# Performance work log

Hardware: AMD Instinct MI355X
Metric: run time of the kernel (lower is better)

Reference implementation:

```python
import jax, jax.numpy as jnp
import numpy as np

N = 8192      # nodes
E = 262144    # edges (avg degree 32)
IN_DIM = 512
H1 = 256
H2 = 128


def _graph_conv(x, src, dst, W, b, act):
    """DGL GraphConv with norm='both', allow_zero_in_degree=True.
    h = D_in^{-1/2} * A @ (D_out^{-1/2} * x @ W) + b, then activation.
    Degrees clamped to min 1 (DGL behavior)."""
    ones = jnp.ones((src.shape[0],), dtype=x.dtype)
    deg_out = jax.ops.segment_sum(ones, src, num_segments=N)
    deg_in = jax.ops.segment_sum(ones, dst, num_segments=N)
    norm_src = jnp.maximum(deg_out, 1.0) ** -0.5  # [N]
    norm_dst = jnp.maximum(deg_in, 1.0) ** -0.5   # [N]
    # apply weight before aggregation (out_feats < in_feats, as DGL does)
    h = (x * norm_src[:, None]) @ W               # [N, out]
    agg = jax.ops.segment_sum(h[src], dst, num_segments=N)  # gather-scatter SpMM
    return act(agg * norm_dst[:, None] + b)


def setup_inputs() -> dict:
    key = jax.random.key(0)
    ks = jax.random.split(key, 7)
    features = jax.random.normal(ks[0], (N, IN_DIM), dtype=jnp.float32)
    src = jax.random.randint(ks[1], (E,), 0, N)
    dst = jax.random.randint(ks[2], (E,), 0, N)
    W1 = jax.random.normal(ks[3], (IN_DIM, H1), dtype=jnp.float32) * (1.0 / np.sqrt(IN_DIM))
    b1 = jnp.zeros((H1,), dtype=jnp.float32)
    W2 = jax.random.normal(ks[4], (H1, H2), dtype=jnp.float32) * (1.0 / np.sqrt(H1))
    b2 = jnp.zeros((H2,), dtype=jnp.float32)
    return {"features": features, "src": src, "dst": dst,
            "W1": W1, "b1": b1, "W2": W2, "b2": b2}


def reference(features, src, dst, W1, b1, W2, b2):
    x = _graph_conv(features, src, dst, W1, b1, jax.nn.relu)
    emb = _graph_conv(x, src, dst, W2, b2, lambda a: a)
    logits = jax.nn.sigmoid(emb @ emb.T)  # [N, N] dense reconstruction
    return (emb, logits)
```

## Files before the change

### kernel.cpp

```cpp
#include <hip/hip_runtime.h>

#define NN 8192
#define EE 262144
#define IN_DIM 512
#define HD1 256
#define HD2 128

typedef __attribute__((ext_vector_type(8))) short bf16x8;
typedef __attribute__((ext_vector_type(4))) float f32x4;

__device__ inline unsigned short f2bf(float f) {
    unsigned int u = __builtin_bit_cast(unsigned int, f);
    u += 0x7fffu + ((u >> 16) & 1u);
    return (unsigned short)(u >> 16);
}


__global__ void deg_kernel(const int* __restrict__ src, const int* __restrict__ dst,
                           int* __restrict__ deg_out, int* __restrict__ deg_in) {
    int e = blockIdx.x * blockDim.x + threadIdx.x;
    if (e < EE) {
        atomicAdd(&deg_out[src[e]], 1);
        atomicAdd(&deg_in[dst[e]], 1);
    }
}

__global__ void norm_kernel(const int* __restrict__ deg_out, const int* __restrict__ deg_in,
                            float* __restrict__ norm_src, float* __restrict__ norm_dst) {
    int i = blockIdx.x * blockDim.x + threadIdx.x;
    if (i < NN) {
        int dout = deg_out[i]; if (dout < 1) dout = 1;
        int din  = deg_in[i];  if (din  < 1) din  = 1;
        norm_src[i] = rsqrtf((float)dout);
        norm_dst[i] = rsqrtf((float)din);
    }
}

__global__ void scan_kernel(const int* __restrict__ counts, int* __restrict__ row_start) {
    __shared__ int sums[256];
    int t = threadIdx.x;
    int base = t * 32;
    int local[32];
    int s = 0;
    for (int i = 0; i < 32; i++) { local[i] = s; s += counts[base + i]; }
    sums[t] = s;
    __syncthreads();
    for (int off = 1; off < 256; off <<= 1) {
        int v = (t >= off) ? sums[t - off] : 0;
        __syncthreads();
        sums[t] += v;
        __syncthreads();
    }
    int coff = (t == 0) ? 0 : sums[t - 1];
    for (int i = 0; i < 32; i++) row_start[base + i] = coff + local[i];
    if (t == 255) row_start[NN] = sums[255];
}

__global__ void fill_kernel(const int* __restrict__ src, const int* __restrict__ dst,
                            const int* __restrict__ row_start, int* __restrict__ cursor,
                            int* __restrict__ eidx) {
    int e = blockIdx.x * blockDim.x + threadIdx.x;
    if (e < EE) {
        int d = dst[e];
        int pos = atomicAdd(&cursor[d], 1);
        eidx[row_start[d] + pos] = src[e];
    }
}


__global__ void scale_cast_kernel(const float4* __restrict__ x, const float* __restrict__ norm_src,
                                  ushort4* __restrict__ out) {
    int idx = blockIdx.x * blockDim.x + threadIdx.x;
    if (idx < NN * IN_DIM / 4) {
        float ns = norm_src[idx >> 7];
        float4 v = x[idx];
        ushort4 o;
        o.x = f2bf(v.x * ns); o.y = f2bf(v.y * ns);
        o.z = f2bf(v.z * ns); o.w = f2bf(v.w * ns);
        out[idx] = o;
    }
}

__global__ void transpose_cast_kernel(const float* __restrict__ W, unsigned short* __restrict__ Wt,
                                      int K, int Nc) {
    int idx = blockIdx.x * blockDim.x + threadIdx.x;
    if (idx < K * Nc) {
        int n = idx / K;
        int k = idx - n * K;
        Wt[idx] = f2bf(W[k * Nc + n]);
    }
}

template <int EPI>
__global__ __launch_bounds__(256) void gemm_tn(const short* __restrict__ A,
                                               const short* __restrict__ B,
                                               float* __restrict__ C, int N, int K) {
    __shared__ float lds[64][132];
    int wave = threadIdx.x >> 6;
    int lane = threadIdx.x & 63;
    int wr = wave >> 1, wc = wave & 1;
    int row0 = blockIdx.y * 128 + wr * 64;
    int col0 = blockIdx.x * 128 + wc * 64;
    int l15 = lane & 15, q = lane >> 4;

    f32x4 acc[4][4] = {};
    const short* Abase = A + (size_t)(row0 + l15) * K + q * 8;
    const short* Bbase = B + (size_t)(col0 + l15) * K + q * 8;
    int nk = K >> 5;
    for (int ks = 0; ks < nk; ks++) {
        bf16x8 a[4], b[4];
#pragma unroll
        for (int t = 0; t < 4; t++) {
            a[t] = *(const bf16x8*)(Abase + (size_t)t * 16 * K + ks * 32);
            b[t] = *(const bf16x8*)(Bbase + (size_t)t * 16 * K + ks * 32);
        }
#pragma unroll
        for (int ti = 0; ti < 4; ti++)
#pragma unroll
            for (int tj = 0; tj < 4; tj++)
                acc[ti][tj] = __builtin_amdgcn_mfma_f32_16x16x32_bf16(a[ti], b[tj], acc[ti][tj], 0, 0, 0);
    }

    int brow = blockIdx.y * 128;
    int bcol = blockIdx.x * 128;
#pragma unroll
    for (int h = 0; h < 2; h++) {
        __syncthreads();
        if (wr == h) {
#pragma unroll
            for (int ti = 0; ti < 4; ti++)
#pragma unroll
                for (int tj = 0; tj < 4; tj++)
#pragma unroll
                    for (int r = 0; r < 4; r++)
                        lds[ti * 16 + q * 4 + r][wc * 64 + tj * 16 + l15] = acc[ti][tj][r];
        }
        __syncthreads();
#pragma unroll
        for (int it = 0; it < 8; it++) {
            int idx = it * 256 + threadIdx.x;
            int rl = idx >> 5;
            int c4 = (idx & 31) << 2;
            f32x4 v = *(const f32x4*)&lds[rl][c4];
            float* dst = C + (size_t)(brow + h * 64 + rl) * N + bcol + c4;
            if (EPI == 1) {
                f32x4 s;
                s[0] = __builtin_amdgcn_rcpf(1.0f + __expf(-v[0]));
                s[1] = __builtin_amdgcn_rcpf(1.0f + __expf(-v[1]));
                s[2] = __builtin_amdgcn_rcpf(1.0f + __expf(-v[2]));
                s[3] = __builtin_amdgcn_rcpf(1.0f + __expf(-v[3]));
                __builtin_nontemporal_store(s, (f32x4*)dst);
            } else {
                *(f32x4*)dst = v;
            }
        }
    }
}


__global__ __launch_bounds__(256) void spmm1_kernel(
        const float* __restrict__ h1, const int* __restrict__ row_start,
        const int* __restrict__ eidx, const float* __restrict__ norm_dst,
        const float* __restrict__ norm_src, const float* __restrict__ b1,
        unsigned short* __restrict__ x1n) {
    int wave = threadIdx.x >> 6, lane = threadIdx.x & 63;
    int r = blockIdx.x * 4 + wave;
    int s = row_start[r], e = row_start[r + 1];
    const float* hb = h1 + (size_t)lane * 4;
    float sx = 0.f, sy = 0.f, sz = 0.f, sw = 0.f;
    int i = s;
    for (; i + 4 <= e; i += 4) {
        int n0 = eidx[i], n1 = eidx[i + 1], n2 = eidx[i + 2], n3 = eidx[i + 3];
        float4 v0 = *(const float4*)(hb + (size_t)n0 * HD1);
        float4 v1 = *(const float4*)(hb + (size_t)n1 * HD1);
        float4 v2 = *(const float4*)(hb + (size_t)n2 * HD1);
        float4 v3 = *(const float4*)(hb + (size_t)n3 * HD1);
        sx += (v0.x + v1.x) + (v2.x + v3.x);
        sy += (v0.y + v1.y) + (v2.y + v3.y);
        sz += (v0.z + v1.z) + (v2.z + v3.z);
        sw += (v0.w + v1.w) + (v2.w + v3.w);
    }
    for (; i < e; i++) {
        float4 v = *(const float4*)(hb + (size_t)eidx[i] * HD1);
        sx += v.x; sy += v.y; sz += v.z; sw += v.w;
    }
    float nd = norm_dst[r], ns = norm_src[r];
    float4 bb = *(const float4*)(b1 + lane * 4);
    ushort4 o;
    o.x = f2bf(fmaxf(sx * nd + bb.x, 0.f) * ns);
    o.y = f2bf(fmaxf(sy * nd + bb.y, 0.f) * ns);
    o.z = f2bf(fmaxf(sz * nd + bb.z, 0.f) * ns);
    o.w = f2bf(fmaxf(sw * nd + bb.w, 0.f) * ns);
    *(ushort4*)(x1n + (size_t)r * HD1 + lane * 4) = o;
}

__global__ __launch_bounds__(256) void spmm2_kernel(
        const float* __restrict__ h2, const int* __restrict__ row_start,
        const int* __restrict__ eidx, const float* __restrict__ norm_dst,
        const float* __restrict__ b2, float* __restrict__ emb,
        unsigned short* __restrict__ embb) {
    int wave = threadIdx.x >> 6, lane = threadIdx.x & 63;
    int r = blockIdx.x * 4 + wave;
    int s = row_start[r], e = row_start[r + 1];
    const float* hb = h2 + (size_t)lane * 2;
    float sx = 0.f, sy = 0.f;
    int i = s;
    for (; i + 4 <= e; i += 4) {
        int n0 = eidx[i], n1 = eidx[i + 1], n2 = eidx[i + 2], n3 = eidx[i + 3];
        float2 v0 = *(const float2*)(hb + (size_t)n0 * HD2);
        float2 v1 = *(const float2*)(hb + (size_t)n1 * HD2);
        float2 v2 = *(const float2*)(hb + (size_t)n2 * HD2);
        float2 v3 = *(const float2*)(hb + (size_t)n3 * HD2);
        sx += (v0.x + v1.x) + (v2.x + v3.x);
        sy += (v0.y + v1.y) + (v2.y + v3.y);
    }
    for (; i < e; i++) {
        float2 v = *(const float2*)(hb + (size_t)eidx[i] * HD2);
        sx += v.x; sy += v.y;
    }
    float nd = norm_dst[r];
    float2 bb = *(const float2*)(b2 + lane * 2);
    float x0 = sx * nd + bb.x;
    float x1 = sy * nd + bb.y;
    float2 ov; ov.x = x0; ov.y = x1;
    *(float2*)(emb + (size_t)r * HD2 + lane * 2) = ov;
    ushort2 ob; ob.x = f2bf(x0); ob.y = f2bf(x1);
    *(ushort2*)(embb + (size_t)r * HD2 + lane * 2) = ob;
}


extern "C" void kernel_launch(void* const* d_in, const int* in_sizes, int n_in,
                              void* d_out, int out_size, void* d_ws, size_t ws_size,
                              hipStream_t stream) {
    const float* features = (const float*)d_in[0];
    const int* src = (const int*)d_in[1];
    const int* dst = (const int*)d_in[2];
    const float* W1 = (const float*)d_in[3];
    const float* b1 = (const float*)d_in[4];
    const float* W2 = (const float*)d_in[5];
    const float* b2 = (const float*)d_in[6];

    char* ws = (char*)d_ws;
    size_t o = 0;
    auto alloc = [&](size_t bytes) -> char* {
        char* p = ws + o;
        o = (o + bytes + 255) & ~(size_t)255;
        return p;
    };
    int* deg_out = (int*)alloc(NN * 4);
    int* deg_in  = (int*)alloc(NN * 4);
    int* cursor  = (int*)alloc(NN * 4);
    float* norm_src = (float*)alloc(NN * 4);
    float* norm_dst = (float*)alloc(NN * 4);
    int* row_start  = (int*)alloc((NN + 1) * 4);
    int* eidx       = (int*)alloc(EE * 4);
    unsigned short* xn  = (unsigned short*)alloc((size_t)NN * IN_DIM * 2);
    unsigned short* w1t = (unsigned short*)alloc((size_t)HD1 * IN_DIM * 2);
    unsigned short* w2t = (unsigned short*)alloc((size_t)HD2 * HD1 * 2);
    float* h1 = (float*)alloc((size_t)NN * HD1 * 4);
    unsigned short* x1n = (unsigned short*)alloc((size_t)NN * HD1 * 2);
    float* h2 = (float*)alloc((size_t)NN * HD2 * 4);
    unsigned short* embb = (unsigned short*)alloc((size_t)NN * HD2 * 2);

    float* emb_out = (float*)d_out;
    float* logits_out = emb_out + (size_t)NN * HD2;

    (void)hipMemsetAsync(deg_out, 0, (size_t)NN * 4 * 3, stream);

    deg_kernel<<<EE / 256, 256, 0, stream>>>(src, dst, deg_out, deg_in);
    norm_kernel<<<NN / 256, 256, 0, stream>>>(deg_out, deg_in, norm_src, norm_dst);
    scan_kernel<<<1, 256, 0, stream>>>(deg_in, row_start);
    fill_kernel<<<EE / 256, 256, 0, stream>>>(src, dst, row_start, cursor, eidx);

    scale_cast_kernel<<<(NN * IN_DIM / 4) / 256, 256, 0, stream>>>(
        (const float4*)features, norm_src, (ushort4*)xn);
    transpose_cast_kernel<<<(IN_DIM * HD1 + 255) / 256, 256, 0, stream>>>(W1, w1t, IN_DIM, HD1);
    transpose_cast_kernel<<<(HD1 * HD2 + 255) / 256, 256, 0, stream>>>(W2, w2t, HD1, HD2);

    gemm_tn<0><<<dim3(HD1 / 128, NN / 128), 256, 0, stream>>>(
        (const short*)xn, (const short*)w1t, h1, HD1, IN_DIM);
    spmm1_kernel<<<NN / 4, 256, 0, stream>>>(h1, row_start, eidx, norm_dst, norm_src, b1, x1n);

    gemm_tn<0><<<dim3(HD2 / 128, NN / 128), 256, 0, stream>>>(
        (const short*)x1n, (const short*)w2t, h2, HD2, HD1);
    spmm2_kernel<<<NN / 4, 256, 0, stream>>>(h2, row_start, eidx, norm_dst, b2, emb_out, embb);

    gemm_tn<1><<<dim3(NN / 128, NN / 128), 256, 0, stream>>>(
        (const short*)embb, (const short*)embb, logits_out, NN, HD2);
}
```

Baseline: 428.5 us.

## Fuse preprocessing kernels and fold feature scaling into first GEMM

Merges degree counting with the weight transpose-casts into one launch, and merges norm computation into the scan kernel. The first GEMM now reads fp32 features directly, converts to bf16 in-register and applies the per-row source norm in the epilogue, which removes the separate scale/cast pass and its intermediate buffer. The small GEMMs use 64-row tiles to launch more blocks on the narrow outputs. Scaling after the bf16 rounding instead of before changes rounding slightly, and the in-loop fp32 loads double the A-operand traffic of GEMM1.

```diff
diff --git a/kernel.cpp b/kernel.cpp
--- a/kernel.cpp
+++ b/kernel.cpp
@@ -15,34 +15,44 @@
     return (unsigned short)(u >> 16);
 }
 
-
-__global__ void deg_kernel(const int* __restrict__ src, const int* __restrict__ dst,
-                           int* __restrict__ deg_out, int* __restrict__ deg_in) {
-    int e = blockIdx.x * blockDim.x + threadIdx.x;
-    if (e < EE) {
+__global__ void prep1_kernel(const int* __restrict__ src, const int* __restrict__ dst,
+                             int* __restrict__ deg_out, int* __restrict__ deg_in,
+                             const float* __restrict__ W1, unsigned short* __restrict__ w1t,
+                             const float* __restrict__ W2, unsigned short* __restrict__ w2t) {
+    int b = blockIdx.x;
+    if (b < 1024) {
+        int e = b * 256 + threadIdx.x;
         atomicAdd(&deg_out[src[e]], 1);
         atomicAdd(&deg_in[dst[e]], 1);
-    }
-}
-
-__global__ void norm_kernel(const int* __restrict__ deg_out, const int* __restrict__ deg_in,
-                            float* __restrict__ norm_src, float* __restrict__ norm_dst) {
-    int i = blockIdx.x * blockDim.x + threadIdx.x;
-    if (i < NN) {
-        int dout = deg_out[i]; if (dout < 1) dout = 1;
-        int din  = deg_in[i];  if (din  < 1) din  = 1;
-        norm_src[i] = rsqrtf((float)dout);
-        norm_dst[i] = rsqrtf((float)din);
-    }
-}
-
-__global__ void scan_kernel(const int* __restrict__ counts, int* __restrict__ row_start) {
+    } else if (b < 1536) {
+        int idx = (b - 1024) * 256 + threadIdx.x;
+        int n = idx / IN_DIM;
+        int k = idx - n * IN_DIM;
+        w1t[idx] = f2bf(W1[k * HD1 + n]);
+    } else {
+        int idx = (b - 1536) * 256 + threadIdx.x;
+        int n = idx / HD1;
+        int k = idx - n * HD1;
+        w2t[idx] = f2bf(W2[k * HD2 + n]);
+    }
+}
+
+__global__ void scan_norm_kernel(const int* __restrict__ deg_in, const int* __restrict__ deg_out,
+                                 int* __restrict__ row_start,
+                                 float* __restrict__ norm_src, float* __restrict__ norm_dst) {
     __shared__ int sums[256];
     int t = threadIdx.x;
     int base = t * 32;
     int local[32];
     int s = 0;
-    for (int i = 0; i < 32; i++) { local[i] = s; s += counts[base + i]; }
+    for (int i = 0; i < 32; i++) {
+        int c = deg_in[base + i];
+        local[i] = s; s += c;
+        int din = (c < 1) ? 1 : c;
+        int dout = deg_out[base + i]; if (dout < 1) dout = 1;
+        norm_dst[base + i] = rsqrtf((float)din);
+        norm_src[base + i] = rsqrtf((float)dout);
+    }
     sums[t] = s;
     __syncthreads();
     for (int off = 1; off < 256; off <<= 1) {
@@ -67,73 +77,67 @@
     }
 }
 
-
-__global__ void scale_cast_kernel(const float4* __restrict__ x, const float* __restrict__ norm_src,
-                                  ushort4* __restrict__ out) {
-    int idx = blockIdx.x * blockDim.x + threadIdx.x;
-    if (idx < NN * IN_DIM / 4) {
-        float ns = norm_src[idx >> 7];
-        float4 v = x[idx];
-        ushort4 o;
-        o.x = f2bf(v.x * ns); o.y = f2bf(v.y * ns);
-        o.z = f2bf(v.z * ns); o.w = f2bf(v.w * ns);
-        out[idx] = o;
-    }
-}
-
-__global__ void transpose_cast_kernel(const float* __restrict__ W, unsigned short* __restrict__ Wt,
-                                      int K, int Nc) {
-    int idx = blockIdx.x * blockDim.x + threadIdx.x;
-    if (idx < K * Nc) {
-        int n = idx / K;
-        int k = idx - n * K;
-        Wt[idx] = f2bf(W[k * Nc + n]);
-    }
-}
-
-template <int EPI>
-__global__ __launch_bounds__(256) void gemm_tn(const short* __restrict__ A,
+template <int TM, int EPI, int AF32>
+__global__ __launch_bounds__(256) void gemm_tn(const void* __restrict__ Av,
                                                const short* __restrict__ B,
-                                               float* __restrict__ C, int N, int K) {
+                                               float* __restrict__ C,
+                                               const float* __restrict__ rowscale,
+                                               int N, int K) {
     __shared__ float lds[64][132];
     int wave = threadIdx.x >> 6;
     int lane = threadIdx.x & 63;
     int wr = wave >> 1, wc = wave & 1;
-    int row0 = blockIdx.y * 128 + wr * 64;
+    int l15 = lane & 15, q = lane >> 4;
+    int row0 = blockIdx.y * (32 * TM) + wr * (16 * TM);
     int col0 = blockIdx.x * 128 + wc * 64;
-    int l15 = lane & 15, q = lane >> 4;
-
-    f32x4 acc[4][4] = {};
-    const short* Abase = A + (size_t)(row0 + l15) * K + q * 8;
-    const short* Bbase = B + (size_t)(col0 + l15) * K + q * 8;
+
+    f32x4 acc[TM][4] = {};
+    const short* Ab = (const short*)Av + (size_t)(row0 + l15) * K + q * 8;
+    const float* Af = (const float*)Av + (size_t)(row0 + l15) * K + q * 8;
+    const short* Bb = B + (size_t)(col0 + l15) * K + q * 8;
     int nk = K >> 5;
     for (int ks = 0; ks < nk; ks++) {
-        bf16x8 a[4], b[4];
-#pragma unroll
-        for (int t = 0; t < 4; t++) {
-            a[t] = *(const bf16x8*)(Abase + (size_t)t * 16 * K + ks * 32);
-            b[t] = *(const bf16x8*)(Bbase + (size_t)t * 16 * K + ks * 32);
+        bf16x8 a[TM], b[4];
+#pragma unroll
+        for (int t = 0; t < TM; t++) {
+            if (AF32) {
+                f32x4 f0 = *(const f32x4*)(Af + (size_t)t * 16 * K + ks * 32);
+                f32x4 f1 = *(const f32x4*)(Af + (size_t)t * 16 * K + ks * 32 + 4);
+                bf16x8 av;
+                av[0] = (short)f2bf(f0[0]); av[1] = (short)f2bf(f0[1]);
+                av[2] = (short)f2bf(f0[2]); av[3] = (short)f2bf(f0[3]);
+                av[4] = (short)f2bf(f1[0]); av[5] = (short)f2bf(f1[1]);
+                av[6] = (short)f2bf(f1[2]); av[7] = (short)f2bf(f1[3]);
+                a[t] = av;
+            } else {
+                a[t] = *(const bf16x8*)(Ab + (size_t)t * 16 * K + ks * 32);
+            }
         }
 #pragma unroll
-        for (int ti = 0; ti < 4; ti++)
+        for (int t = 0; t < 4; t++)
+            b[t] = *(const bf16x8*)(Bb + (size_t)t * 16 * K + ks * 32);
+#pragma unroll
+        for (int ti = 0; ti < TM; ti++)
 #pragma unroll
             for (int tj = 0; tj < 4; tj++)
                 acc[ti][tj] = __builtin_amdgcn_mfma_f32_16x16x32_bf16(a[ti], b[tj], acc[ti][tj], 0, 0, 0);
     }
 
-    int brow = blockIdx.y * 128;
+    int brow = blockIdx.y * (32 * TM);
     int bcol = blockIdx.x * 128;
-#pragma unroll
-    for (int h = 0; h < 2; h++) {
-        __syncthreads();
-        if (wr == h) {
-#pragma unroll
-            for (int ti = 0; ti < 4; ti++)
+    constexpr int PH = (32 * TM) / 64;
+#pragma unroll
+    for (int h = 0; h < PH; h++) {
+        __syncthreads();
+        if (PH == 1 || wr == h) {
+            int rbase = (PH == 1) ? wr * (16 * TM) : 0;
+#pragma unroll
+            for (int ti = 0; ti < TM; ti++)
 #pragma unroll
                 for (int tj = 0; tj < 4; tj++)
 #pragma unroll
                     for (int r = 0; r < 4; r++)
-                        lds[ti * 16 + q * 4 + r][wc * 64 + tj * 16 + l15] = acc[ti][tj][r];
+                        lds[rbase + ti * 16 + q * 4 + r][wc * 64 + tj * 16 + l15] = acc[ti][tj][r];
         }
         __syncthreads();
 #pragma unroll
@@ -142,7 +146,8 @@
             int rl = idx >> 5;
             int c4 = (idx & 31) << 2;
             f32x4 v = *(const f32x4*)&lds[rl][c4];
-            float* dst = C + (size_t)(brow + h * 64 + rl) * N + bcol + c4;
+            int grow = brow + h * 64 + rl;
+            float* dst = C + (size_t)grow * N + bcol + c4;
             if (EPI == 1) {
                 f32x4 s;
                 s[0] = __builtin_amdgcn_rcpf(1.0f + __expf(-v[0]));
@@ -150,6 +155,10 @@
                 s[2] = __builtin_amdgcn_rcpf(1.0f + __expf(-v[2]));
                 s[3] = __builtin_amdgcn_rcpf(1.0f + __expf(-v[3]));
                 __builtin_nontemporal_store(s, (f32x4*)dst);
+            } else if (EPI == 2) {
+                float ns = rowscale[grow];
+                v[0] *= ns; v[1] *= ns; v[2] *= ns; v[3] *= ns;
+                *(f32x4*)dst = v;
             } else {
                 *(f32x4*)dst = v;
             }
@@ -254,7 +263,6 @@
     float* norm_dst = (float*)alloc(NN * 4);
     int* row_start  = (int*)alloc((NN + 1) * 4);
     int* eidx       = (int*)alloc(EE * 4);
-    unsigned short* xn  = (unsigned short*)alloc((size_t)NN * IN_DIM * 2);
     unsigned short* w1t = (unsigned short*)alloc((size_t)HD1 * IN_DIM * 2);
     unsigned short* w2t = (unsigned short*)alloc((size_t)HD2 * HD1 * 2);
     float* h1 = (float*)alloc((size_t)NN * HD1 * 4);
@@ -267,24 +275,18 @@
 
     (void)hipMemsetAsync(deg_out, 0, (size_t)NN * 4 * 3, stream);
 
-    deg_kernel<<<EE / 256, 256, 0, stream>>>(src, dst, deg_out, deg_in);
-    norm_kernel<<<NN / 256, 256, 0, stream>>>(deg_out, deg_in, norm_src, norm_dst);
-    scan_kernel<<<1, 256, 0, stream>>>(deg_in, row_start);
+    prep1_kernel<<<1664, 256, 0, stream>>>(src, dst, deg_out, deg_in, W1, w1t, W2, w2t);
+    scan_norm_kernel<<<1, 256, 0, stream>>>(deg_in, deg_out, row_start, norm_src, norm_dst);
     fill_kernel<<<EE / 256, 256, 0, stream>>>(src, dst, row_start, cursor, eidx);
 
-    scale_cast_kernel<<<(NN * IN_DIM / 4) / 256, 256, 0, stream>>>(
-        (const float4*)features, norm_src, (ushort4*)xn);
-    transpose_cast_kernel<<<(IN_DIM * HD1 + 255) / 256, 256, 0, stream>>>(W1, w1t, IN_DIM, HD1);
-    transpose_cast_kernel<<<(HD1 * HD2 + 255) / 256, 256, 0, stream>>>(W2, w2t, HD1, HD2);
-
-    gemm_tn<0><<<dim3(HD1 / 128, NN / 128), 256, 0, stream>>>(
-        (const short*)xn, (const short*)w1t, h1, HD1, IN_DIM);
+    gemm_tn<2, 2, 1><<<dim3(HD1 / 128, NN / 64), 256, 0, stream>>>(
+        (const void*)features, (const short*)w1t, h1, norm_src, HD1, IN_DIM);
     spmm1_kernel<<<NN / 4, 256, 0, stream>>>(h1, row_start, eidx, norm_dst, norm_src, b1, x1n);
 
-    gemm_tn<0><<<dim3(HD2 / 128, NN / 128), 256, 0, stream>>>(
-        (const short*)x1n, (const short*)w2t, h2, HD2, HD1);
+    gemm_tn<2, 0, 0><<<dim3(HD2 / 128, NN / 64), 256, 0, stream>>>(
+        (const void*)x1n, (const short*)w2t, h2, nullptr, HD2, HD1);
     spmm2_kernel<<<NN / 4, 256, 0, stream>>>(h2, row_start, eidx, norm_dst, b2, emb_out, embb);
 
-    gemm_tn<1><<<dim3(NN / 128, NN / 128), 256, 0, stream>>>(
-        (const short*)embb, (const short*)embb, logits_out, NN, HD2);
-}
+    gemm_tn<4, 1, 0><<<dim3(NN / 128, NN / 128), 256, 0, stream>>>(
+        (const void*)embb, (const short*)embb, logits_out, nullptr, NN, HD2);
+}
```

New measurement: 418.9 us. -2.2%, faster.
